# Optimization experiments

Hardware: AMD Instinct MI355X
Metric: run time of the kernel (lower is better)

Reference implementation:

```python
import jax, jax.numpy as jnp
import numpy as np

BLOCK_SIZE = 4096
EMBED_SIZE = 1024
HEAD_SIZE = 128


def setup_inputs() -> dict:
    key = jax.random.key(0)
    kx, kq, kk, kv = jax.random.split(key, 4)
    B, T = 8, BLOCK_SIZE
    x = jax.random.normal(kx, (B, T, EMBED_SIZE), dtype=jnp.float32)
    # nn.Linear(embed, head, bias=False): weight (head, embed); y = x @ W.T
    scale = 1.0 / np.sqrt(EMBED_SIZE)
    Wq = jax.random.uniform(kq, (HEAD_SIZE, EMBED_SIZE), dtype=jnp.float32, minval=-scale, maxval=scale)
    Wk = jax.random.uniform(kk, (HEAD_SIZE, EMBED_SIZE), dtype=jnp.float32, minval=-scale, maxval=scale)
    Wv = jax.random.uniform(kv, (HEAD_SIZE, EMBED_SIZE), dtype=jnp.float32, minval=-scale, maxval=scale)
    return {"x": x, "Wq": Wq, "Wk": Wk, "Wv": Wv}


def reference(x, Wq, Wk, Wv):
    B, T, C = x.shape
    q = jnp.einsum('btc,hc->bth', x, Wq)  # (B,T,H)
    k = jnp.einsum('btc,hc->bth', x, Wk)
    v = jnp.einsum('btc,hc->bth', x, Wv)
    scale = jnp.asarray(Wq.shape[0], x.dtype) ** -0.5
    wei = jnp.einsum('bth,bsh->bts', q, k) * scale  # (B,T,T)
    causal = jnp.tril(jnp.ones((T, T), dtype=bool))
    wei = jnp.where(causal, wei, -jnp.inf)
    wei = jax.nn.softmax(wei, axis=-1)
    out = jnp.einsum('bts,bsh->bth', wei, v)  # (B,T,H)
    return out
```

## Files before the change

kernel.cpp:

```cpp
#include <hip/hip_runtime.h>
#include <stdint.h>

typedef unsigned short u16;
typedef __attribute__((ext_vector_type(8))) short short8;
typedef __attribute__((ext_vector_type(4))) float f32x4;

#define B_ 8
#define T_ 4096
#define C_ 1024
#define H_ 128

#if __has_builtin(__builtin_amdgcn_exp2f)
#define EXP2(x) __builtin_amdgcn_exp2f(x)
#else
#define EXP2(x) exp2f(x)
#endif

__device__ __forceinline__ u16 f2bf(float f) {
  union { float f; uint32_t u; } v; v.f = f;
  uint32_t r = v.u + 0x7fffu + ((v.u >> 16) & 1u);
  return (u16)(r >> 16);
}

__device__ __forceinline__ u16 f2bf_rn(float f) {
  union { float f; uint32_t u; } v; v.f = f;
  return (u16)((v.u + 0x8000u) >> 16);
}

__device__ __forceinline__ void gl_lds16(const u16* g, u16* l) {
  __builtin_amdgcn_global_load_lds(
      (const __attribute__((address_space(1))) void*)g,
      (__attribute__((address_space(3))) void*)l, 16, 0, 0);
}

__global__ __launch_bounds__(256) void wconv_kernel(
    const float* __restrict__ Wq, const float* __restrict__ Wk,
    const float* __restrict__ Wv, u16* __restrict__ Wb) {
  int g = (blockIdx.x * 256 + threadIdx.x) * 8;
  int head = g >> 17;
  int off  = g & 131071;
  const float* W = (head == 0) ? Wq : (head == 1) ? Wk : Wv;
  float s = (head == 0) ? 0.12751743342f : 1.0f;
  float4 a = *(const float4*)(W + off);
  float4 b = *(const float4*)(W + off + 4);
  u16 o[8] = {f2bf(a.x * s), f2bf(a.y * s), f2bf(a.z * s), f2bf(a.w * s),
              f2bf(b.x * s), f2bf(b.y * s), f2bf(b.z * s), f2bf(b.w * s)};
  *(uint4*)(Wb + g) = *(const uint4*)o;
}

__global__ __launch_bounds__(512) void proj_kernel(
    const float* __restrict__ x, const u16* __restrict__ Wb,
    u16* __restrict__ qo, u16* __restrict__ ko, u16* __restrict__ vto) {
  __shared__ u16 Xl[64 * 72];
  __shared__ u16 Wl[384 * 72];

  const int bm   = blockIdx.x;
  const int tid  = threadIdx.x;
  const int wave = tid >> 6;
  const int lane = tid & 63;
  const int m    = lane & 15;
  const int q4   = lane >> 4;
  const int rowg = wave & 1;
  const int colg = wave >> 1;

  f32x4 acc[12] = {};

  const int xrow = tid >> 3, xc8 = (tid & 7) * 8;

  for (int kc = 0; kc < C_; kc += 64) {
    __syncthreads();
    {
      const float* xp = x + (size_t)(bm * 64 + xrow) * C_ + kc + xc8;
      float4 a = *(const float4*)xp;
      float4 b = *(const float4*)(xp + 4);
      u16 o[8] = {f2bf(a.x), f2bf(a.y), f2bf(a.z), f2bf(a.w),
                  f2bf(b.x), f2bf(b.y), f2bf(b.z), f2bf(b.w)};
      *(uint4*)&Xl[xrow * 72 + xc8] = *(const uint4*)o;
    }
    #pragma unroll
    for (int i = 0; i < 6; ++i) {
      int g = i * 512 + tid;
      int row = g >> 3, c8 = (g & 7) * 8;
      *(uint4*)&Wl[row * 72 + c8] =
          *(const uint4*)(Wb + (size_t)row * C_ + kc + c8);
    }
    __syncthreads();

    #pragma unroll
    for (int kb = 0; kb < 2; ++kb) {
      short8 af0 = *(const short8*)&Xl[(rowg * 32 + m) * 72 + kb * 32 + q4 * 8];
      short8 af1 = *(const short8*)&Xl[(rowg * 32 + 16 + m) * 72 + kb * 32 + q4 * 8];
      #pragma unroll
      for (int nb = 0; nb < 6; ++nb) {
        short8 bf = *(const short8*)&Wl[(colg * 96 + nb * 16 + m) * 72 + kb * 32 + q4 * 8];
        acc[nb]     = __builtin_amdgcn_mfma_f32_16x16x32_bf16(af0, bf, acc[nb], 0, 0, 0);
        acc[6 + nb] = __builtin_amdgcn_mfma_f32_16x16x32_bf16(af1, bf, acc[6 + nb], 0, 0, 0);
      }
    }
  }

  #pragma unroll
  for (int half = 0; half < 2; ++half) {
    const int rowoff = rowg * 32 + half * 16 + q4 * 4;
    #pragma unroll
    for (int nb = 0; nb < 6; ++nb) {
      int col = colg * 96 + nb * 16 + m;
      f32x4 a = acc[half * 6 + nb];
      if (col < 128) {
        #pragma unroll
        for (int r = 0; r < 4; ++r)
          qo[(size_t)(bm * 64 + rowoff + r) * H_ + col] = f2bf(a[r]);
      } else if (col < 256) {
        #pragma unroll
        for (int r = 0; r < 4; ++r)
          ko[(size_t)(bm * 64 + rowoff + r) * H_ + (col - 128)] = f2bf(a[r]);
      } else {
        int b = bm >> 6;
        int t = (bm & 63) * 64 + rowoff;
        u16* vp = vto + (size_t)b * H_ * T_ + (size_t)(col - 256) * T_ + t;
        #pragma unroll
        for (int r = 0; r < 4; ++r) vp[r] = f2bf(a[r]);
      }
    }
  }
}

__global__ __launch_bounds__(256, 2) void attn_kernel(
    const u16* __restrict__ q, const u16* __restrict__ k,
    const u16* __restrict__ vt, float* __restrict__ out,
    float* __restrict__ po, float* __restrict__ pl) {
  __shared__ u16 Kl[2][64 * 128];
  __shared__ u16 Vl[2][128 * 64];
  __shared__ u16 Pl[4][2][16 * 64];

  const int bid   = blockIdx.x;
  const int batch = bid & 7;
  const int c     = bid >> 3;
  int Q, ck;
  if (c < 24)      { Q = 31 - c / 3;        ck = c % 3; }
  else if (c < 40) { Q = 23 - (c - 24) / 2; ck = (c - 24) & 1; }
  else if (c < 48) { Q = 15 - (c - 40);     ck = 0; }
  else { int t = c - 48; int qm = 7 - (t >> 2);
         Q = qm + (t & 3) * 8; ck = Q >> 3; }
  const int k0   = ck * 16;
  const int kend = min(k0 + 16, 2 * Q + 2);
  const bool single = (Q < 8);

  const int tid  = threadIdx.x;
  const int wave = tid >> 6;
  const int lane = tid & 63;
  const int m    = lane & 15;
  const int q4   = lane >> 4;

  const size_t bbase = (size_t)batch * T_ * H_;
  const u16* vbase   = vt + (size_t)batch * H_ * T_;

  short8 qf[2][4];
  #pragma unroll
  for (int si = 0; si < 2; ++si) {
    const u16* qp = q + bbase + (size_t)(Q * 128 + wave * 32 + si * 16 + m) * H_;
    #pragma unroll
    for (int kb = 0; kb < 4; ++kb)
      qf[si][kb] = *(const short8*)(qp + kb * 32 + q4 * 8);
  }

  const u16* gK[4];
  const u16* gV[4];
  #pragma unroll
  for (int j = 0; j < 4; ++j) {
    int r = wave * 16 + j * 4 + (lane >> 4);
    gK[j] = k + bbase + (size_t)r * H_ + (((lane & 15) ^ (r & 7)) << 3);
    int h = wave * 32 + j * 8 + (lane >> 3);
    gV[j] = vbase + (size_t)h * T_ + (((lane & 7) ^ (h & 7)) << 3);
  }

#define STAGE(bi, KT)                                                         \
  {                                                                           \
    u16* kd = &Kl[bi][wave * 16 * 128];                                       \
    const size_t ko_ = (size_t)(KT) * (64 * H_);                              \
    _Pragma("unroll") for (int j = 0; j < 4; ++j)                             \
        gl_lds16(gK[j] + ko_, kd + j * 4 * 128);                              \
    u16* vd = &Vl[bi][wave * 32 * 64];                                        \
    const size_t vo_ = (size_t)(KT) * 64;                                     \
    _Pragma("unroll") for (int j = 0; j < 4; ++j)                             \
        gl_lds16(gV[j] + vo_, vd + j * 8 * 64);                               \
  }

  float li[2][4] = {};
  f32x4 o[2][8] = {};
  const float NEGINF = -__builtin_inff();

  STAGE(0, k0);
  __syncthreads();
  int cur = 0;

  for (int kt = k0; kt < kend; ++kt) {
    if (kt + 1 < kend) STAGE(cur ^ 1, kt + 1);

    f32x4 sv[2][4];
    __builtin_amdgcn_s_setprio(1);
    #pragma unroll
    for (int nb = 0; nb < 4; ++nb) {
      f32x4 a0 = {}, a1 = {};
      #pragma unroll
      for (int kb = 0; kb < 4; ++kb) {
        short8 kf = *(const short8*)&Kl[cur][(nb * 16 + m) * 128 +
                                             (((kb * 4 + q4) ^ (m & 7)) << 3)];
        a0 = __builtin_amdgcn_mfma_f32_16x16x32_bf16(qf[0][kb], kf, a0, 0, 0, 0);
        a1 = __builtin_amdgcn_mfma_f32_16x16x32_bf16(qf[1][kb], kf, a1, 0, 0, 0);
      }
      sv[0][nb] = a0; sv[1][nb] = a1;
    }
    __builtin_amdgcn_s_setprio(0);

    if ((kt >> 1) == Q) {
      #pragma unroll
      for (int si = 0; si < 2; ++si)
        #pragma unroll
        for (int nb = 0; nb < 4; ++nb)
          #pragma unroll
          for (int r = 0; r < 4; ++r) {
            int key = ((kt & 1) << 6) + nb * 16 + m;
            int row = wave * 32 + si * 16 + q4 * 4 + r;
            if (key > row) sv[si][nb][r] = NEGINF;
          }
    }

    #pragma unroll
    for (int si = 0; si < 2; ++si)
      #pragma unroll
      for (int nb = 0; nb < 4; ++nb)
        #pragma unroll
        for (int r = 0; r < 4; ++r) {
          float p = EXP2(sv[si][nb][r]);
          li[si][r] += p;
          int rr = q4 * 4 + r;
          Pl[wave][si][rr * 64 + (((nb * 2 + (m >> 3)) ^ (rr & 7)) << 3) +
                       (m & 7)] = f2bf_rn(p);
        }

    __asm__ __volatile__("s_waitcnt lgkmcnt(0)" ::: "memory");
    __builtin_amdgcn_sched_barrier(0);

    __builtin_amdgcn_s_setprio(1);
    #pragma unroll
    for (int kb2 = 0; kb2 < 2; ++kb2) {
      short8 pf0 = *(const short8*)&Pl[wave][0][m * 64 +
                                   (((kb2 * 4 + q4) ^ (m & 7)) << 3)];
      short8 pf1 = *(const short8*)&Pl[wave][1][m * 64 +
                                   (((kb2 * 4 + q4) ^ (m & 7)) << 3)];
      #pragma unroll
      for (int nb = 0; nb < 8; ++nb) {
        short8 vf = *(const short8*)&Vl[cur][(nb * 16 + m) * 64 +
                                             (((kb2 * 4 + q4) ^ (m & 7)) << 3)];
        o[0][nb] = __builtin_amdgcn_mfma_f32_16x16x32_bf16(pf0, vf, o[0][nb], 0, 0, 0);
        o[1][nb] = __builtin_amdgcn_mfma_f32_16x16x32_bf16(pf1, vf, o[1][nb], 0, 0, 0);
      }
    }
    __builtin_amdgcn_s_setprio(0);

    if (kt + 1 < kend) {
      __syncthreads();
      cur ^= 1;
    }
  }

  #pragma unroll
  for (int si = 0; si < 2; ++si)
    #pragma unroll
    for (int r = 0; r < 4; ++r) {
      float t0 = li[si][r];
      t0 += __shfl_xor(t0, 1, 64);
      t0 += __shfl_xor(t0, 2, 64);
      t0 += __shfl_xor(t0, 4, 64);
      t0 += __shfl_xor(t0, 8, 64);
      li[si][r] = t0;
    }

  if (single) {
    #pragma unroll
    for (int si = 0; si < 2; ++si) {
      float* op = out + bbase + (size_t)(Q * 128 + wave * 32 + si * 16) * H_;
      #pragma unroll
      for (int nb = 0; nb < 8; ++nb)
        #pragma unroll
        for (int r = 0; r < 4; ++r)
          op[(q4 * 4 + r) * H_ + nb * 16 + m] = o[si][nb][r] / li[si][r];
    }
  } else {
    const size_t slot = (size_t)(batch * 32 + Q) * 4 + ck;
    #pragma unroll
    for (int si = 0; si < 2; ++si) {
      float* pp = po + slot * 16384 + (size_t)(wave * 32 + si * 16) * 128;
      #pragma unroll
      for (int nb = 0; nb < 8; ++nb)
        #pragma unroll
        for (int r = 0; r < 4; ++r)
          pp[(q4 * 4 + r) * 128 + nb * 16 + m] = o[si][nb][r];
      if (m == 0) {
        #pragma unroll
        for (int r = 0; r < 4; ++r)
          pl[slot * 128 + wave * 32 + si * 16 + q4 * 4 + r] = li[si][r];
      }
    }
  }
}

__global__ __launch_bounds__(256) void combine_kernel(
    const float* __restrict__ po, const float* __restrict__ pl,
    float* __restrict__ out) {
  int gid = blockIdx.x * 256 + threadIdx.x;
  int h4  = (gid & 31) * 4;
  int tt  = (gid >> 5) & 4095;
  int b   = gid >> 17;
  int Q   = tt >> 7, row = tt & 127;
  if (Q < 8) return;
  int nc = (Q >> 3) + 1;
  float4 s = {0.f, 0.f, 0.f, 0.f};
  float l = 0.f;
  for (int ck = 0; ck < nc; ++ck) {
    size_t slot = (size_t)(b * 32 + Q) * 4 + ck;
    float4 p = *(const float4*)(po + slot * 16384 + row * 128 + h4);
    s.x += p.x; s.y += p.y; s.z += p.z; s.w += p.w;
    l += pl[slot * 128 + row];
  }
  float inv = 1.0f / l;
  float4 r; r.x = s.x * inv; r.y = s.y * inv; r.z = s.z * inv; r.w = s.w * inv;
  *(float4*)(out + ((size_t)b * T_ + tt) * H_ + h4) = r;
}

extern "C" void kernel_launch(void* const* d_in, const int* in_sizes, int n_in,
                              void* d_out, int out_size, void* d_ws,
                              size_t ws_size, hipStream_t stream) {
  const float* x  = (const float*)d_in[0];
  const float* Wq = (const float*)d_in[1];
  const float* Wk = (const float*)d_in[2];
  const float* Wv = (const float*)d_in[3];

  const size_t n = (size_t)B_ * T_ * H_;
  u16* qb  = (u16*)d_ws;
  u16* kb  = qb + n;
  u16* vtb = kb + n;
  u16* Wbb = vtb + n;
  float* po = (float*)(Wbb + 393216);
  float* pl = po + (size_t)1024 * 16384;

  wconv_kernel<<<dim3(192), dim3(256), 0, stream>>>(Wq, Wk, Wv, Wbb);
  proj_kernel<<<dim3(512), dim3(512), 0, stream>>>(x, Wbb, qb, kb, vtb);
  attn_kernel<<<dim3(640), dim3(256), 0, stream>>>(qb, kb, vtb, (float*)d_out, po, pl);
  combine_kernel<<<dim3(4096), dim3(256), 0, stream>>>(po, pl, (float*)d_out);
}
```

Baseline: 279.2 us.

## Restructure projection kernel to 4 waves with direct-to-LDS swizzled weight loads

The projection kernel drops from 8 to 4 waves per block. Each wave now computes all 64 rows against its own 96 output columns, so every weight fragment read from LDS feeds four MFMAs instead of two. Weight tiles are copied global-to-LDS with async 16-byte loads into an unpadded, XOR-swizzled layout, which removes the register round trip and shrinks LDS use. X loads are widened to 16 floats per thread. The cost is a larger accumulator footprint (24 f32x4 per thread), which may limit occupancy despite the launch-bounds hint of two blocks per CU.

```diff
diff --git a/kernel.cpp b/kernel.cpp
--- a/kernel.cpp
+++ b/kernel.cpp
@@ -48,11 +48,11 @@
   *(uint4*)(Wb + g) = *(const uint4*)o;
 }
 
-__global__ __launch_bounds__(512) void proj_kernel(
+__global__ __launch_bounds__(256, 2) void proj_kernel(
     const float* __restrict__ x, const u16* __restrict__ Wb,
     u16* __restrict__ qo, u16* __restrict__ ko, u16* __restrict__ vto) {
+  __shared__ u16 Wl[384 * 64];
   __shared__ u16 Xl[64 * 72];
-  __shared__ u16 Wl[384 * 72];
 
   const int bm   = blockIdx.x;
   const int tid  = threadIdx.x;
@@ -60,52 +60,59 @@
   const int lane = tid & 63;
   const int m    = lane & 15;
   const int q4   = lane >> 4;
-  const int rowg = wave & 1;
-  const int colg = wave >> 1;
-
-  f32x4 acc[12] = {};
-
-  const int xrow = tid >> 3, xc8 = (tid & 7) * 8;
+
+  f32x4 acc[4][6] = {};
+
+  const int xrow = tid >> 2, xc16 = (tid & 3) * 16;
+  const u16* gW = Wb + (size_t)(wave * 96 + (lane >> 3)) * C_ +
+                  (((lane & 7) ^ (lane >> 3)) << 3);
+  const float* gX = x + (size_t)(bm * 64 + xrow) * C_ + xc16;
 
   for (int kc = 0; kc < C_; kc += 64) {
     __syncthreads();
+    #pragma unroll
+    for (int j = 0; j < 12; ++j)
+      gl_lds16(gW + kc + (size_t)(j * 8) * C_, &Wl[(wave * 96 + j * 8) * 64]);
     {
-      const float* xp = x + (size_t)(bm * 64 + xrow) * C_ + kc + xc8;
+      const float* xp = gX + kc;
       float4 a = *(const float4*)xp;
       float4 b = *(const float4*)(xp + 4);
-      u16 o[8] = {f2bf(a.x), f2bf(a.y), f2bf(a.z), f2bf(a.w),
-                  f2bf(b.x), f2bf(b.y), f2bf(b.z), f2bf(b.w)};
-      *(uint4*)&Xl[xrow * 72 + xc8] = *(const uint4*)o;
-    }
-    #pragma unroll
-    for (int i = 0; i < 6; ++i) {
-      int g = i * 512 + tid;
-      int row = g >> 3, c8 = (g & 7) * 8;
-      *(uint4*)&Wl[row * 72 + c8] =
-          *(const uint4*)(Wb + (size_t)row * C_ + kc + c8);
+      float4 c = *(const float4*)(xp + 8);
+      float4 d = *(const float4*)(xp + 12);
+      u16 o[16] = {f2bf_rn(a.x), f2bf_rn(a.y), f2bf_rn(a.z), f2bf_rn(a.w),
+                   f2bf_rn(b.x), f2bf_rn(b.y), f2bf_rn(b.z), f2bf_rn(b.w),
+                   f2bf_rn(c.x), f2bf_rn(c.y), f2bf_rn(c.z), f2bf_rn(c.w),
+                   f2bf_rn(d.x), f2bf_rn(d.y), f2bf_rn(d.z), f2bf_rn(d.w)};
+      *(uint4*)&Xl[xrow * 72 + xc16]     = *(const uint4*)&o[0];
+      *(uint4*)&Xl[xrow * 72 + xc16 + 8] = *(const uint4*)&o[8];
     }
     __syncthreads();
 
     #pragma unroll
     for (int kb = 0; kb < 2; ++kb) {
-      short8 af0 = *(const short8*)&Xl[(rowg * 32 + m) * 72 + kb * 32 + q4 * 8];
-      short8 af1 = *(const short8*)&Xl[(rowg * 32 + 16 + m) * 72 + kb * 32 + q4 * 8];
+      short8 af[4];
+      #pragma unroll
+      for (int s = 0; s < 4; ++s)
+        af[s] = *(const short8*)&Xl[(s * 16 + m) * 72 + kb * 32 + q4 * 8];
       #pragma unroll
       for (int nb = 0; nb < 6; ++nb) {
-        short8 bf = *(const short8*)&Wl[(colg * 96 + nb * 16 + m) * 72 + kb * 32 + q4 * 8];
-        acc[nb]     = __builtin_amdgcn_mfma_f32_16x16x32_bf16(af0, bf, acc[nb], 0, 0, 0);
-        acc[6 + nb] = __builtin_amdgcn_mfma_f32_16x16x32_bf16(af1, bf, acc[6 + nb], 0, 0, 0);
+        short8 bf = *(const short8*)&Wl[(wave * 96 + nb * 16 + m) * 64 +
+                                        (((kb * 4 + q4) ^ (m & 7)) << 3)];
+        #pragma unroll
+        for (int s = 0; s < 4; ++s)
+          acc[s][nb] =
+              __builtin_amdgcn_mfma_f32_16x16x32_bf16(af[s], bf, acc[s][nb], 0, 0, 0);
       }
     }
   }
 
   #pragma unroll
-  for (int half = 0; half < 2; ++half) {
-    const int rowoff = rowg * 32 + half * 16 + q4 * 4;
+  for (int s = 0; s < 4; ++s) {
+    const int rowoff = s * 16 + q4 * 4;
     #pragma unroll
     for (int nb = 0; nb < 6; ++nb) {
-      int col = colg * 96 + nb * 16 + m;
-      f32x4 a = acc[half * 6 + nb];
+      int col = wave * 96 + nb * 16 + m;
+      f32x4 a = acc[s][nb];
       if (col < 128) {
         #pragma unroll
         for (int r = 0; r < 4; ++r)
@@ -346,7 +353,7 @@
   float* pl = po + (size_t)1024 * 16384;
 
   wconv_kernel<<<dim3(192), dim3(256), 0, stream>>>(Wq, Wk, Wv, Wbb);
-  proj_kernel<<<dim3(512), dim3(512), 0, stream>>>(x, Wbb, qb, kb, vtb);
+  proj_kernel<<<dim3(512), dim3(256), 0, stream>>>(x, Wbb, qb, kb, vtb);
   attn_kernel<<<dim3(640), dim3(256), 0, stream>>>(qb, kb, vtb, (float*)d_out, po, pl);
   combine_kernel<<<dim3(4096), dim3(256), 0, stream>>>(po, pl, (float*)d_out);
 }
```

New measurement: 277.9 us. Within noise of the previous version (-0.5%).
